# Performance work log

Hardware: AMD Instinct MI355X
Metric: run time of the kernel (lower is better)

## Reference

```python
import jax, jax.numpy as jnp
import numpy as np

S, B, D, H, V, TOK = 512, 32, 512, 512, 64, 30000
L = 2  # num LSTM layers


def _lstm_dir(x, Wih, Whh, bih, bhh, reverse):
    # x: [S, B, Din]; Wih: [4H, Din]; Whh: [4H, H]
    Bn = x.shape[1]
    Hn = Whh.shape[1]

    def step(carry, xt):
        h, c = carry
        g = xt @ Wih.T + h @ Whh.T + bih + bhh  # [B, 4H]
        i, f, gg, o = jnp.split(g, 4, axis=-1)  # torch gate order i,f,g,o
        c = jax.nn.sigmoid(f) * c + jax.nn.sigmoid(i) * jnp.tanh(gg)
        h = jax.nn.sigmoid(o) * jnp.tanh(c)
        return (h, c), h

    init = (jnp.zeros((Bn, Hn), x.dtype), jnp.zeros((Bn, Hn), x.dtype))
    _, hs = jax.lax.scan(step, init, x, reverse=reverse)
    return hs  # [S, B, H], time-aligned with x


def _bilstm(x, Wih0, Whh0, bih0, bhh0, Wih1, Whh1, bih1, bhh1):
    # layer 0
    hf = _lstm_dir(x, Wih0[0], Whh0[0], bih0[0], bhh0[0], reverse=False)
    hb = _lstm_dir(x, Wih0[1], Whh0[1], bih0[1], bhh0[1], reverse=True)
    x = jnp.concatenate([hf, hb], axis=-1)  # [S, B, 2H]
    # layer 1
    hf = _lstm_dir(x, Wih1[0], Whh1[0], bih1[0], bhh1[0], reverse=False)
    hb = _lstm_dir(x, Wih1[1], Whh1[1], bih1[1], bhh1[1], reverse=True)
    return jnp.concatenate([hf, hb], axis=-1)  # [S, B, 2H]


def setup_inputs() -> dict:
    key = jax.random.key(0)
    ks = jax.random.split(key, 16)
    s = 0.05
    inp = {}
    inp['source'] = jax.random.randint(ks[0], (S, B), 0, TOK)
    inp['target'] = jax.random.randint(ks[1], (S, B), 0, V)
    inp['emb'] = jax.random.normal(ks[2], (TOK, D), jnp.float32) * s
    inp['Wih0'] = jax.random.normal(ks[3], (2, 4 * H, D), jnp.float32) * s
    inp['Whh0'] = jax.random.normal(ks[4], (2, 4 * H, H), jnp.float32) * s
    inp['bih0'] = jax.random.normal(ks[5], (2, 4 * H), jnp.float32) * s
    inp['bhh0'] = jax.random.normal(ks[6], (2, 4 * H), jnp.float32) * s
    inp['Wih1'] = jax.random.normal(ks[7], (2, 4 * H, 2 * H), jnp.float32) * s
    inp['Whh1'] = jax.random.normal(ks[8], (2, 4 * H, H), jnp.float32) * s
    inp['bih1'] = jax.random.normal(ks[9], (2, 4 * H), jnp.float32) * s
    inp['bhh1'] = jax.random.normal(ks[10], (2, 4 * H), jnp.float32) * s
    inp['Wout'] = jax.random.normal(ks[11], (V, 2 * H), jnp.float32) * s
    inp['bout'] = jax.random.normal(ks[12], (V,), jnp.float32) * s
    inp['trans'] = jax.random.uniform(ks[13], (V, V), jnp.float32)  # torch.rand
    return inp


def reference(source, target, emb, Wih0, Whh0, bih0, bhh0, Wih1, Whh1, bih1, bhh1, Wout, bout, trans):
    # get_logits: frozen embedding -> BiLSTM -> linear
    x = jax.lax.stop_gradient(emb[source])  # [S, B, D] (embedding under no_grad)
    h = _bilstm(x, Wih0, Whh0, bih0, bhh0, Wih1, Whh1, bih1, bhh1)  # [S, B, 2H]
    logits = (h @ Wout.T + bout)[:, 0, :]  # [S, V] -- forward() decodes batch 0

    # Viterbi: max-plus recurrence over time
    def vstep(delta, lt):
        scores = delta[:, None] + trans + lt[None, :]  # [V_prev, V_cur]
        return jnp.max(scores, axis=0), jnp.argmax(scores, axis=0)

    delta, bps = jax.lax.scan(vstep, logits[0], logits[1:])  # bps: [S-1, V]
    last = jnp.argmax(delta)

    def back(idx, bp):
        prev = bp[idx]
        return prev, prev

    _, rev = jax.lax.scan(back, last, bps, reverse=True)  # rev[t] = tag at t, t in [0, S-2]
    path = jnp.concatenate([rev, last[None]]).astype(jnp.int32)  # [S]
    return path
```

## Files before the change

kernel.cpp:

```cpp
#include <hip/hip_runtime.h>
#include <stdint.h>

constexpr int kS = 512;
constexpr int kB = 32;
constexpr int kH = 512;
constexpr int kV = 64;


__device__ __forceinline__ float fast_sigmoid(float x) {
  return __builtin_amdgcn_rcpf(1.0f + __expf(-x));
}
__device__ __forceinline__ float fast_tanh(float x) {
  return 1.0f - 2.0f * __builtin_amdgcn_rcpf(1.0f + __expf(2.0f * x));
}
__device__ __forceinline__ float bcast(float v, int k) {
  return __uint_as_float(__builtin_amdgcn_readlane(__float_as_uint(v), k));
}

__global__ __launch_bounds__(128) void k_embed(const int* __restrict__ src,
                                               const float* __restrict__ emb,
                                               float* __restrict__ X) {
  const int t = blockIdx.x;
  const int s = src[t * kB];
  const float4* e = (const float4*)(emb + (size_t)s * 512);
  float4* x = (float4*)(X + (size_t)t * 512);
  x[threadIdx.x] = e[threadIdx.x];
}

template <int KZ>
__global__ __launch_bounds__(512, 1) void k_rec(
    const float* __restrict__ Z0,
    const float* __restrict__ Z1,
    const float* __restrict__ Wih,
    const float* __restrict__ Whh,
    const float* __restrict__ bih,
    const float* __restrict__ bhh,
    float* __restrict__ Hout) {
  constexpr int ZPW = KZ / 8;
  __shared__ float part[64 * 9];
  const int bx = blockIdx.x;
  const int dir = bx & 1, wg = bx >> 1;
  const int tid = threadIdx.x;
  const int wv = tid >> 6, l = tid & 63;
  const float* WihB = Wih + (size_t)dir * 2048 * KZ;
  const float* WhhB = Whh + (size_t)dir * 2048 * 512;
  float* Hb = Hout + (size_t)dir * kS * kH;
  const int grow = (l >> 4) * 512 + wg * 16 + (l & 15);

  float ww[64];
  {
    const float* wp = WhhB + (size_t)grow * 512 + wv * 64;
#pragma unroll
    for (int i = 0; i < 64; i += 4) {
      const float4 v = *(const float4*)(wp + i);
      ww[i] = v.x; ww[i + 1] = v.y; ww[i + 2] = v.z; ww[i + 3] = v.w;
    }
  }
  float zw[ZPW];
  {
    const float* zp = WihB + (size_t)grow * KZ + wv * ZPW;
#pragma unroll
    for (int i = 0; i < ZPW; i += 4) {
      const float4 v = *(const float4*)(zp + i);
      zw[i] = v.x; zw[i + 1] = v.y; zw[i + 2] = v.z; zw[i + 3] = v.w;
    }
  }
  float bias = 0.0f;
  if (wv == 0) bias = bih[dir * 2048 + grow] + bhh[dir * 2048 + grow];
  float cstate = 0.0f;

  const float* zbase = (KZ == 512) ? Z0 : ((wv < 4) ? Z0 : Z1);
  const int zoff = (KZ == 512) ? tid : ((wv & 3) * 128 + l);

  const int t0 = dir ? (kS - 1) : 0;
  float zc0 = zbase[(size_t)t0 * 512 + zoff];
  float zc1 = (KZ == 1024) ? zbase[(size_t)t0 * 512 + zoff + 64] : 0.0f;

  for (int s = 0; s < kS; s++) {
    const int t = dir ? (kS - 1 - s) : s;
    int tn = dir ? (t - 1) : (t + 1);
    if (tn < 0) tn = 0;
    if (tn > kS - 1) tn = kS - 1;
    const float zn0 = zbase[(size_t)tn * 512 + zoff];
    const float zn1 = (KZ == 1024) ? zbase[(size_t)tn * 512 + zoff + 64] : 0.0f;

    float a0 = 0.f, a1 = 0.f, a2 = 0.f, a3 = 0.f;
#pragma unroll
    for (int k = 0; k < 64; k += 4) {
      a0 += zw[k + 0] * bcast(zc0, k + 0);
      a1 += zw[k + 1] * bcast(zc0, k + 1);
      a2 += zw[k + 2] * bcast(zc0, k + 2);
      a3 += zw[k + 3] * bcast(zc0, k + 3);
    }
    if (KZ == 1024) {
#pragma unroll
      for (int k = 0; k < 64; k += 4) {
        a0 += zw[64 + k + 0] * bcast(zc1, k + 0);
        a1 += zw[64 + k + 1] * bcast(zc1, k + 1);
        a2 += zw[64 + k + 2] * bcast(zc1, k + 2);
        a3 += zw[64 + k + 3] * bcast(zc1, k + 3);
      }
    }

    float hreg = 0.0f;
    if (s > 0) {
      const int tp = dir ? (t + 1) : (t - 1);
      const unsigned* hp = (const unsigned*)(Hb + (size_t)tp * kH) + tid;
      unsigned u;
      do {
        u = __hip_atomic_load(hp, __ATOMIC_RELAXED, __HIP_MEMORY_SCOPE_AGENT);
      } while (u == 0xFFFFFFFFu);
      hreg = __uint_as_float(u);
    }

#pragma unroll
    for (int k = 0; k < 64; k += 4) {
      a0 += ww[k + 0] * bcast(hreg, k + 0);
      a1 += ww[k + 1] * bcast(hreg, k + 1);
      a2 += ww[k + 2] * bcast(hreg, k + 2);
      a3 += ww[k + 3] * bcast(hreg, k + 3);
    }
    part[l * 9 + wv] = (a0 + a1) + (a2 + a3);
    __syncthreads();
    if (wv == 0) {
      float ssum = bias;
#pragma unroll
      for (int w = 0; w < 8; w++) ssum += part[l * 9 + w];
      const float sf = __shfl(ssum, (l + 16) & 63);
      const float sg = __shfl(ssum, (l + 32) & 63);
      const float so = __shfl(ssum, (l + 48) & 63);
      if (l < 16) {
        const float ig = fast_sigmoid(ssum);
        const float fg = fast_sigmoid(sf);
        const float og = fast_sigmoid(so);
        cstate = fg * cstate + ig * fast_tanh(sg);
        const float h = og * fast_tanh(cstate);
        __hip_atomic_store((unsigned*)(Hb + (size_t)t * kH) + wg * 16 + l,
                           __float_as_uint(h), __ATOMIC_RELAXED,
                           __HIP_MEMORY_SCOPE_AGENT);
      }
    }
    zc0 = zn0;
    zc1 = zn1;
  }
}

__global__ __launch_bounds__(256) void k_logits(const float* __restrict__ H1,
                                                const float* __restrict__ Wout,
                                                const float* __restrict__ bout,
                                                float* __restrict__ LOG) {
  __shared__ float hl[1024];
  const int t = blockIdx.x;
  const int tid = threadIdx.x;
  float4* hl4 = (float4*)hl;
  if (tid < 128)
    hl4[tid] = ((const float4*)(H1 + (size_t)t * kH))[tid];
  else
    hl4[tid] = ((const float4*)(H1 + (size_t)(kS + t) * kH))[tid - 128];
  __syncthreads();
  const int v = tid >> 2, q = tid & 3;
  const float4* w4 = (const float4*)(Wout + (size_t)v * 1024);
  float4 a = {0, 0, 0, 0};
#pragma unroll 8
  for (int j = 0; j < 64; j++) {
    const int idx = j * 4 + q;
    const float4 w = w4[idx];
    const float4 x = hl4[idx];
    a.x += w.x * x.x; a.y += w.y * x.y; a.z += w.z * x.z; a.w += w.w * x.w;
  }
  float acc = (a.x + a.y) + (a.z + a.w);
  acc += __shfl_xor(acc, 1);
  acc += __shfl_xor(acc, 2);
  if (q == 0) LOG[(size_t)t * kV + v] = acc + bout[v];
}

__global__ __launch_bounds__(256) void k_viterbi(const float* __restrict__ LOG,
                                                 const float* __restrict__ trans,
                                                 int* __restrict__ out) {
  __shared__ float delta[64];
  __shared__ float redS[4 * 64];
  __shared__ int redA[4 * 64];
  __shared__ unsigned char bp[511 * 64];
  const int tid = threadIdx.x;
  const int c = tid & 63, q = tid >> 6;
  if (tid < 64) delta[tid] = LOG[tid];
  __syncthreads();
  for (int t = 1; t < kS; t++) {
    float best = -1e30f;
    int bi = 0;
#pragma unroll 4
    for (int pp = 0; pp < 16; pp++) {
      const int p = q * 16 + pp;
      const float sc = delta[p] + trans[p * 64 + c];
      if (sc > best) { best = sc; bi = p; }
    }
    redS[q * 64 + c] = best;
    redA[q * 64 + c] = bi;
    __syncthreads();
    if (tid < 64) {
      float b = redS[c];
      int a = redA[c];
      for (int qq = 1; qq < 4; qq++) {
        const float v2 = redS[qq * 64 + c];
        if (v2 > b) { b = v2; a = redA[qq * 64 + c]; }
      }
      bp[(t - 1) * 64 + c] = (unsigned char)a;
      delta[c] = b + LOG[t * 64 + c];
    }
    __syncthreads();
  }
  if (tid == 0) {
    float b = delta[0];
    int a = 0;
    for (int i = 1; i < 64; i++)
      if (delta[i] > b) { b = delta[i]; a = i; }
    int idx = a;
    out[kS - 1] = idx;
    for (int t = kS - 2; t >= 0; t--) {
      idx = bp[t * 64 + idx];
      out[t] = idx;
    }
  }
}

extern "C" void kernel_launch(void* const* d_in, const int* in_sizes, int n_in,
                              void* d_out, int out_size, void* d_ws,
                              size_t ws_size, hipStream_t stream) {
  (void)in_sizes; (void)n_in; (void)out_size; (void)ws_size;
  const int* source  = (const int*)d_in[0];
  const float* emb   = (const float*)d_in[2];
  const float* Wih0  = (const float*)d_in[3];
  const float* Whh0  = (const float*)d_in[4];
  const float* bih0  = (const float*)d_in[5];
  const float* bhh0  = (const float*)d_in[6];
  const float* Wih1  = (const float*)d_in[7];
  const float* Whh1  = (const float*)d_in[8];
  const float* bih1  = (const float*)d_in[9];
  const float* bhh1  = (const float*)d_in[10];
  const float* Wout  = (const float*)d_in[11];
  const float* bout  = (const float*)d_in[12];
  const float* trans = (const float*)d_in[13];

  float* ws = (float*)d_ws;
  float* X   = ws;
  float* H0  = ws + 262144;
  float* H1  = ws + 786432;
  float* LOG = ws + 1310720;

  hipMemsetAsync(H0, 0xFF, (size_t)1048576 * sizeof(float), stream);

  k_embed<<<kS, 128, 0, stream>>>(source, emb, X);
  k_rec<512><<<64, 512, 0, stream>>>(X, X, Wih0, Whh0, bih0, bhh0, H0);
  k_rec<1024><<<64, 512, 0, stream>>>(H0, H0 + 262144, Wih1, Whh1, bih1, bhh1, H1);
  k_logits<<<kS, 256, 0, stream>>>(H1, Wout, bout, LOG);
  k_viterbi<<<1, 256, 0, stream>>>(LOG, trans, (int*)d_out);
}
```

Baseline: 2.111 ms.

## Place recurrence blocks on one XCD and exchange hidden state via local L2

The grid grows to 256 blocks and only blocks with blockIdx mod 8 in {0,1} do work. Under round-robin dispatch across the eight XCDs, this should put all working blocks of each direction on the same XCD. Each hidden state is written twice: once with sc0 stores that stay coherent in that XCD's L2, and once with agent-scope atomics. Consumers poll the L2 copy a few times before falling back to the device-coherent copy, aiming to cut the latency of the per-step inter-block handoff. The approach relies on an undocumented block-to-XCD mapping, adds extra stores and memory, and launches 192 idle blocks.

```diff
diff --git a/kernel.cpp b/kernel.cpp
--- a/kernel.cpp
+++ b/kernel.cpp
@@ -15,6 +15,16 @@
 }
 __device__ __forceinline__ float bcast(float v, int k) {
   return __uint_as_float(__builtin_amdgcn_readlane(__float_as_uint(v), k));
+}
+__device__ __forceinline__ unsigned ld_l2(const unsigned* p) {
+  unsigned r;
+  asm volatile("global_load_dword %0, %1, off sc0\n\ts_waitcnt vmcnt(0)"
+               : "=v"(r) : "v"(p) : "memory");
+  return r;
+}
+__device__ __forceinline__ void st_l2(unsigned* p, unsigned v) {
+  asm volatile("global_store_dword %0, %1, off sc0" :: "v"(p), "v"(v)
+               : "memory");
 }
 
 __global__ __launch_bounds__(128) void k_embed(const int* __restrict__ src,
@@ -35,16 +45,20 @@
     const float* __restrict__ Whh,
     const float* __restrict__ bih,
     const float* __restrict__ bhh,
-    float* __restrict__ Hout) {
+    float* __restrict__ HL,
+    float* __restrict__ HG) {
   constexpr int ZPW = KZ / 8;
   __shared__ float part[64 * 9];
-  const int bx = blockIdx.x;
-  const int dir = bx & 1, wg = bx >> 1;
+  const int b = blockIdx.x;
+  const int xslot = b & 7;
+  if (xslot > 1) return;
+  const int dir = xslot, wg = b >> 3;
   const int tid = threadIdx.x;
   const int wv = tid >> 6, l = tid & 63;
   const float* WihB = Wih + (size_t)dir * 2048 * KZ;
   const float* WhhB = Whh + (size_t)dir * 2048 * 512;
-  float* Hb = Hout + (size_t)dir * kS * kH;
+  float* HbL = HL + (size_t)dir * kS * kH;
+  float* HbG = HG + (size_t)dir * kS * kH;
   const int grow = (l >> 4) * 512 + wg * 16 + (l & 15);
 
   float ww[64];
@@ -105,11 +119,16 @@
     float hreg = 0.0f;
     if (s > 0) {
       const int tp = dir ? (t + 1) : (t - 1);
-      const unsigned* hp = (const unsigned*)(Hb + (size_t)tp * kH) + tid;
-      unsigned u;
-      do {
-        u = __hip_atomic_load(hp, __ATOMIC_RELAXED, __HIP_MEMORY_SCOPE_AGENT);
-      } while (u == 0xFFFFFFFFu);
+      const unsigned* lp = (const unsigned*)(HbL + (size_t)tp * kH) + tid;
+      const unsigned* gp = (const unsigned*)(HbG + (size_t)tp * kH) + tid;
+      unsigned u = ld_l2(lp);
+#pragma unroll 1
+      for (int r = 0; r < 4; r++) {
+        if (u != 0xFFFFFFFFu) break;
+        u = ld_l2(lp);
+      }
+      while (u == 0xFFFFFFFFu)
+        u = __hip_atomic_load(gp, __ATOMIC_RELAXED, __HIP_MEMORY_SCOPE_AGENT);
       hreg = __uint_as_float(u);
     }
 
@@ -135,8 +154,11 @@
         const float og = fast_sigmoid(so);
         cstate = fg * cstate + ig * fast_tanh(sg);
         const float h = og * fast_tanh(cstate);
-        __hip_atomic_store((unsigned*)(Hb + (size_t)t * kH) + wg * 16 + l,
-                           __float_as_uint(h), __ATOMIC_RELAXED,
+        const unsigned hv = __float_as_uint(h);
+        unsigned* lq = (unsigned*)(HbL + (size_t)t * kH) + wg * 16 + l;
+        unsigned* gq = (unsigned*)(HbG + (size_t)t * kH) + wg * 16 + l;
+        st_l2(lq, hv);
+        __hip_atomic_store(gq, hv, __ATOMIC_RELAXED,
                            __HIP_MEMORY_SCOPE_AGENT);
       }
     }
@@ -243,15 +265,18 @@
 
   float* ws = (float*)d_ws;
   float* X   = ws;
-  float* H0  = ws + 262144;
-  float* H1  = ws + 786432;
-  float* LOG = ws + 1310720;
-
-  hipMemsetAsync(H0, 0xFF, (size_t)1048576 * sizeof(float), stream);
+  float* H0L = ws + 262144;
+  float* H0G = ws + 786432;
+  float* H1L = ws + 1310720;
+  float* H1G = ws + 1835008;
+  float* LOG = ws + 2359296;
+
+  hipMemsetAsync(H0L, 0xFF, (size_t)4 * 524288 * sizeof(float), stream);
 
   k_embed<<<kS, 128, 0, stream>>>(source, emb, X);
-  k_rec<512><<<64, 512, 0, stream>>>(X, X, Wih0, Whh0, bih0, bhh0, H0);
-  k_rec<1024><<<64, 512, 0, stream>>>(H0, H0 + 262144, Wih1, Whh1, bih1, bhh1, H1);
-  k_logits<<<kS, 256, 0, stream>>>(H1, Wout, bout, LOG);
+  k_rec<512><<<256, 512, 0, stream>>>(X, X, Wih0, Whh0, bih0, bhh0, H0L, H0G);
+  k_rec<1024><<<256, 512, 0, stream>>>(H0G, H0G + 262144, Wih1, Whh1, bih1,
+                                       bhh1, H1L, H1G);
+  k_logits<<<kS, 256, 0, stream>>>(H1G, Wout, bout, LOG);
   k_viterbi<<<1, 256, 0, stream>>>(LOG, trans, (int*)d_out);
 }
```

After: 2.045 ms. 1.03x faster.

## Prefetch previous hidden state early and consume it in 16-lane chunks

Applied to the files above, without the earlier changes.

The load of the previous timestep's hidden state is issued at the start of each step with an inline-asm non-blocking global load using sc0 sc1 cache bits, so it overlaps the input-projection FMAs. The spin-wait is then split into four 16-lane groups, so each wave can start the recurrent FMAs for a quarter of h as soon as that quarter's producer has written it, rather than waiting for all 64 values. The gate activations are also moved to run in parallel across all 64 lanes before the shuffles, which shortens the serial tail on wave 0. The risks are inline asm that depends on vmcnt semantics, and extra ballot and loop overhead in the chunked wait.

```diff
diff --git a/kernel.cpp b/kernel.cpp
--- a/kernel.cpp
+++ b/kernel.cpp
@@ -15,6 +15,20 @@
 }
 __device__ __forceinline__ float bcast(float v, int k) {
   return __uint_as_float(__builtin_amdgcn_readlane(__float_as_uint(v), k));
+}
+__device__ __forceinline__ unsigned ld_mall_nowait(const unsigned* p) {
+  unsigned r;
+  asm volatile("global_load_dword %0, %1, off sc0 sc1" : "=v"(r) : "v"(p));
+  return r;
+}
+__device__ __forceinline__ void wait_vm0(unsigned& r) {
+  asm volatile("s_waitcnt vmcnt(0)" : "+v"(r)::"memory");
+}
+__device__ __forceinline__ unsigned ld_mall(const unsigned* p) {
+  unsigned r;
+  asm volatile("global_load_dword %0, %1, off sc0 sc1\n\ts_waitcnt vmcnt(0)"
+               : "=v"(r) : "v"(p) : "memory");
+  return r;
 }
 
 __global__ __launch_bounds__(128) void k_embed(const int* __restrict__ src,
@@ -81,6 +95,14 @@
     int tn = dir ? (t - 1) : (t + 1);
     if (tn < 0) tn = 0;
     if (tn > kS - 1) tn = kS - 1;
+    int tp = dir ? (t + 1) : (t - 1);
+    if (tp < 0) tp = 0;
+    if (tp > kS - 1) tp = kS - 1;
+    const unsigned* hp = (const unsigned*)(Hb + (size_t)tp * kH) + tid;
+
+    unsigned u = 0;
+    if (s > 0) u = ld_mall_nowait(hp);
+
     const float zn0 = zbase[(size_t)tn * 512 + zoff];
     const float zn1 = (KZ == 1024) ? zbase[(size_t)tn * 512 + zoff + 64] : 0.0f;
 
@@ -102,23 +124,23 @@
       }
     }
 
-    float hreg = 0.0f;
     if (s > 0) {
-      const int tp = dir ? (t + 1) : (t - 1);
-      const unsigned* hp = (const unsigned*)(Hb + (size_t)tp * kH) + tid;
-      unsigned u;
-      do {
-        u = __hip_atomic_load(hp, __ATOMIC_RELAXED, __HIP_MEMORY_SCOPE_AGENT);
-      } while (u == 0xFFFFFFFFu);
-      hreg = __uint_as_float(u);
-    }
-
-#pragma unroll
-    for (int k = 0; k < 64; k += 4) {
-      a0 += ww[k + 0] * bcast(hreg, k + 0);
-      a1 += ww[k + 1] * bcast(hreg, k + 1);
-      a2 += ww[k + 2] * bcast(hreg, k + 2);
-      a3 += ww[k + 3] * bcast(hreg, k + 3);
+      wait_vm0(u);
+#pragma unroll
+      for (int q = 0; q < 4; q++) {
+        const unsigned long long cm = 0xFFFFULL << (q * 16);
+        while (__ballot(u == 0xFFFFFFFFu) & cm) {
+          if (u == 0xFFFFFFFFu) u = ld_mall(hp);
+        }
+        const float hq = __uint_as_float(u);
+#pragma unroll
+        for (int k = q * 16; k < q * 16 + 16; k += 4) {
+          a0 += ww[k + 0] * bcast(hq, k + 0);
+          a1 += ww[k + 1] * bcast(hq, k + 1);
+          a2 += ww[k + 2] * bcast(hq, k + 2);
+          a3 += ww[k + 3] * bcast(hq, k + 3);
+        }
+      }
     }
     part[l * 9 + wv] = (a0 + a1) + (a2 + a3);
     __syncthreads();
@@ -126,14 +148,13 @@
       float ssum = bias;
 #pragma unroll
       for (int w = 0; w < 8; w++) ssum += part[l * 9 + w];
-      const float sf = __shfl(ssum, (l + 16) & 63);
-      const float sg = __shfl(ssum, (l + 32) & 63);
-      const float so = __shfl(ssum, (l + 48) & 63);
+      const float act = (l >= 32 && l < 48) ? fast_tanh(ssum)
+                                            : fast_sigmoid(ssum);
+      const float fg = __shfl(act, (l + 16) & 63);
+      const float gt = __shfl(act, (l + 32) & 63);
+      const float og = __shfl(act, (l + 48) & 63);
       if (l < 16) {
-        const float ig = fast_sigmoid(ssum);
-        const float fg = fast_sigmoid(sf);
-        const float og = fast_sigmoid(so);
-        cstate = fg * cstate + ig * fast_tanh(sg);
+        cstate = fg * cstate + act * gt;
         const float h = og * fast_tanh(cstate);
         __hip_atomic_store((unsigned*)(Hb + (size_t)t * kH) + wg * 16 + l,
                            __float_as_uint(h), __ATOMIC_RELAXED,
```

Result: no change. 2.127 ms (+0.7%).
